# Optimization experiments

Measured on AMD Instinct MI355X. Metric: run time of the kernel, lower is better.

Reference implementation:

```python
import jax, jax.numpy as jnp
import numpy as np

B, S, D, H = 4, 2048, 1024, 16
DK = D // H


def setup_inputs() -> dict:
    key = jax.random.key(0)
    ks = jax.random.split(key, 12)
    std = 0.02
    inp = {
        "query": jax.random.normal(ks[0], (B, S, D), jnp.float32),
        "key": jax.random.normal(ks[1], (B, S, D), jnp.float32),
        "value": jax.random.normal(ks[2], (B, S, D), jnp.float32),
        "mask": jnp.ones((B, 1, 1, S), jnp.int32),
        "Wq": jax.random.normal(ks[3], (D, D), jnp.float32) * std,
        "bq": jnp.zeros((D,), jnp.float32),
        "Wk": jax.random.normal(ks[4], (D, D), jnp.float32) * std,
        "bk": jnp.zeros((D,), jnp.float32),
        "Wv": jax.random.normal(ks[5], (D, D), jnp.float32) * std,
        "bv": jnp.zeros((D,), jnp.float32),
        "Wo": jax.random.normal(ks[6], (D, D), jnp.float32) * std,
        "bo": jnp.zeros((D,), jnp.float32),
    }
    return inp


def reference(query, key, value, mask, Wq, bq, Wk, bk, Wv, bv, Wo, bo):
    # nn.Linear: x @ W.T + b; then split heads -> [B, H, S, DK]
    def proj(x, W, b):
        y = x @ W.T + b
        return y.reshape(B, S, H, DK).transpose(0, 2, 1, 3)

    q = proj(query, Wq, bq)
    k = proj(key, Wk, bk)
    v = proj(value, Wv, bv)

    scale = 1.0 / jnp.sqrt(jnp.asarray(DK, q.dtype))
    scores = jnp.einsum('bhqd,bhkd->bhqk', q, k) * scale  # [B,H,S,S]
    scores = jnp.where(mask == 0, jnp.asarray(-1e9, scores.dtype), scores)
    p_attn = jax.nn.softmax(scores, axis=-1)  # dropout p=0 -> identity
    ctx = jnp.einsum('bhqk,bhkd->bhqd', p_attn, v)
    ctx = ctx.transpose(0, 2, 1, 3).reshape(B, S, D)
    out = ctx @ Wo.T + bo
    return out
```

## Files before the change

### kernel.cpp

```cpp
#include <hip/hip_runtime.h>

#define BB 4
#define SS 2048
#define DD 1024
#define HH 16
#define DKC 64
#define MT (BB*SS)
#define NX (MT*DD)
#define NW (DD*DD)

typedef _Float16 f16x8 __attribute__((ext_vector_type(8)));
typedef _Float16 f16x4 __attribute__((ext_vector_type(4)));
typedef _Float16 f16x2 __attribute__((ext_vector_type(2)));
typedef float f32x4 __attribute__((ext_vector_type(4)));
typedef int   i32x4 __attribute__((ext_vector_type(4)));

__global__ __launch_bounds__(256) void cvt_all(const float* __restrict__ xq,
                                               const float* __restrict__ xk,
                                               const float* __restrict__ xv,
                                               const float* __restrict__ wq,
                                               const float* __restrict__ wk,
                                               const float* __restrict__ wv,
                                               const float* __restrict__ wo,
                                               _Float16* __restrict__ dst) {
  size_t i = ((size_t)blockIdx.x * 256 + threadIdx.x) * 4;
  const float* src; size_t off;
  if (i < (size_t)NX)          { src = xq; off = i; }
  else if (i < (size_t)2*NX)   { src = xk; off = i - (size_t)NX; }
  else if (i < (size_t)3*NX)   { src = xv; off = i - (size_t)2*NX; }
  else {
    size_t j = i - (size_t)3*NX;
    if (j < (size_t)NW)        { src = wq; off = j; }
    else if (j < (size_t)2*NW) { src = wk; off = j - (size_t)NW; }
    else if (j < (size_t)3*NW) { src = wv; off = j - (size_t)2*NW; }
    else                       { src = wo; off = j - (size_t)3*NW; }
  }
  f32x4 f = *(const f32x4*)(src + off);
  f16x4 o;
#pragma unroll
  for (int j = 0; j < 4; ++j) o[j] = (_Float16)f[j];
  *(f16x4*)(dst + i) = o;
}

__global__ __launch_bounds__(256) void gemm_qkv(const _Float16* __restrict__ Xb,
                                                const _Float16* __restrict__ Wb,
                                                const float* __restrict__ b0,
                                                const float* __restrict__ b1,
                                                const float* __restrict__ b2,
                                                _Float16* __restrict__ Pj) {
  const int z = blockIdx.z;
  const _Float16* A = Xb + (size_t)z * MT * DD;
  const _Float16* W = Wb + (size_t)z * DD * DD;
  const float* bias = (z == 0) ? b0 : ((z == 1) ? b1 : b2);
  _Float16* out = Pj + (size_t)z * MT * DD;

  const int m0 = blockIdx.x * 128;
  const int n0 = blockIdx.y * 128;
  const int t = threadIdx.x;
  const int lane = t & 63;
  const int wave = t >> 6;
  const int q = lane >> 4, r = lane & 15;
  const int wm = (wave & 1) * 64, wn = (wave >> 1) * 64;

  __shared__ __align__(16) _Float16 sA[128 * 32];
  __shared__ __align__(16) _Float16 sB[128 * 32];

  f32x4 acc[4][4] = {};

  const int row0 = t >> 2, cc = t & 3;

  f16x8 apre[2], bpre[2];
#pragma unroll
  for (int i = 0; i < 2; ++i) {
    int row = row0 + 64 * i;
    apre[i] = *(const f16x8*)(A + (size_t)(m0 + row) * DD + cc * 8);
    bpre[i] = *(const f16x8*)(W + (size_t)(n0 + row) * DD + cc * 8);
  }

  for (int k0 = 0; k0 < DD; k0 += 32) {
#pragma unroll
    for (int i = 0; i < 2; ++i) {
      int c = t + 256 * i;
      *(f16x8*)&sA[c * 8] = apre[i];
      *(f16x8*)&sB[c * 8] = bpre[i];
    }
    __syncthreads();

    if (k0 + 32 < DD) {
#pragma unroll
      for (int i = 0; i < 2; ++i) {
        int row = row0 + 64 * i;
        apre[i] = *(const f16x8*)(A + (size_t)(m0 + row) * DD + k0 + 32 + cc * 8);
        bpre[i] = *(const f16x8*)(W + (size_t)(n0 + row) * DD + k0 + 32 + cc * 8);
      }
    }

    f16x8 af[4], bf[4];
#pragma unroll
    for (int x = 0; x < 4; ++x) {
      af[x] = *(const f16x8*)&sA[(wm + x * 16 + r) * 32 + q * 8];
      bf[x] = *(const f16x8*)&sB[(wn + x * 16 + r) * 32 + q * 8];
    }
#pragma unroll
    for (int mi = 0; mi < 4; ++mi)
#pragma unroll
      for (int ni = 0; ni < 4; ++ni)
        acc[mi][ni] = __builtin_amdgcn_mfma_f32_16x16x32_f16(af[mi], bf[ni], acc[mi][ni], 0, 0, 0);
    __syncthreads();
  }

  if (z == 2) {
#pragma unroll
    for (int ni = 0; ni < 4; ++ni) {
      int gn = n0 + wn + ni * 16 + r;
      float bv = bias[gn];
      int h = gn >> 6, dk = gn & 63;
#pragma unroll
      for (int mi = 0; mi < 4; ++mi) {
        int gm = m0 + wm + mi * 16 + q * 4;
        int bb = gm >> 11, s0 = gm & 2047;
        int kl = s0 & 63;
        int kap0 = (kl & 15) * 4 + (kl >> 4);
        size_t base = ((size_t)((bb * HH + h) * DKC + dk)) * SS + (s0 - kl);
#pragma unroll
        for (int rr = 0; rr < 4; ++rr)
          out[base + kap0 + rr * 4] = (_Float16)(acc[mi][ni][rr] + bv);
      }
    }
  } else {
#pragma unroll
    for (int ni = 0; ni < 4; ++ni) {
      int gn = n0 + wn + ni * 16 + r;
      float bv = bias[gn];
      int h = gn >> 6, dk = gn & 63;
#pragma unroll
      for (int mi = 0; mi < 4; ++mi) {
#pragma unroll
        for (int rr = 0; rr < 4; ++rr) {
          int gm = m0 + wm + mi * 16 + q * 4 + rr;
          int bb = gm >> 11, s = gm & 2047;
          out[((size_t)((bb * HH + h) * SS + s)) * DKC + dk] = (_Float16)(acc[mi][ni][rr] + bv);
        }
      }
    }
  }
}

__global__ __launch_bounds__(256) void attn(const _Float16* __restrict__ Pj,
                                            const int* __restrict__ mask,
                                            _Float16* __restrict__ Cx) {
  const int qt = blockIdx.x, h = blockIdx.y, bb = blockIdx.z;
  const size_t hoff = ((size_t)(bb * HH + h) * SS) * DKC;
  const _Float16* Qh  = Pj + hoff;
  const _Float16* Kh  = Pj + (size_t)MT * DD + hoff;
  const _Float16* Vth = Pj + (size_t)2 * MT * DD + hoff;
  _Float16* Ch = Cx + hoff;
  const int* mrow = mask + bb * SS;

  const int t = threadIdx.x, lane = t & 63, wave = t >> 6;
  const int q = lane >> 4, r = lane & 15;
  const int qrow0 = qt * 128 + wave * 32;

  __shared__ __align__(16) _Float16 sK[64 * 64];
  __shared__ __align__(16) _Float16 sVt[64 * 64];
  __shared__ __align__(16) _Float16 sP[4][32 * 64];
  __shared__ __align__(16) float    sMB[SS];

  {
    int i0 = t * 8;
    i32x4 m0v = *(const i32x4*)(mrow + i0);
    i32x4 m1v = *(const i32x4*)(mrow + i0 + 4);
    f32x4 b0v, b1v;
#pragma unroll
    for (int j = 0; j < 4; ++j) {
      b0v[j] = m0v[j] ? 0.0f : -1e30f;
      b1v[j] = m1v[j] ? 0.0f : -1e30f;
    }
    *(f32x4*)&sMB[i0] = b0v;
    *(f32x4*)&sMB[i0 + 4] = b1v;
  }

  f16x8 qf[2][2];
#pragma unroll
  for (int mi = 0; mi < 2; ++mi)
#pragma unroll
    for (int kk = 0; kk < 2; ++kk)
      qf[mi][kk] = *(const f16x8*)&Qh[(size_t)(qrow0 + mi * 16 + r) * DKC + kk * 32 + q * 8];

  float lst[2][4] = {};
  f32x4 oacc[2][4] = {};

  const float C2 = 0.125f * 1.44269504089f;

  const int srow0 = t >> 3, scc = t & 7;

  f16x8 kpre[2], vpre[2];
#pragma unroll
  for (int i = 0; i < 2; ++i) {
    int row = srow0 + 32 * i;
    kpre[i] = *(const f16x8*)(Kh + (size_t)row * DKC + scc * 8);
    vpre[i] = *(const f16x8*)(Vth + (size_t)row * SS + scc * 8);
  }

  for (int kt = 0; kt < SS; kt += 64) {
#pragma unroll
    for (int i = 0; i < 2; ++i) {
      int row = srow0 + 32 * i;
      *(f16x8*)&sK [row * 64 + ((scc ^ (row & 7)) << 3)]        = kpre[i];
      *(f16x8*)&sVt[row * 64 + ((scc ^ ((row & 1) << 2)) << 3)] = vpre[i];
    }
    __syncthreads();

    if (kt + 64 < SS) {
#pragma unroll
      for (int i = 0; i < 2; ++i) {
        int row = srow0 + 32 * i;
        kpre[i] = *(const f16x8*)(Kh + (size_t)(kt + 64 + row) * DKC + scc * 8);
        vpre[i] = *(const f16x8*)(Vth + (size_t)row * SS + kt + 64 + scc * 8);
      }
    }

    f32x4 sacc[2][4] = {};
#pragma unroll
    for (int kk = 0; kk < 2; ++kk) {
      f16x8 kb[4];
#pragma unroll
      for (int ni = 0; ni < 4; ++ni)
        kb[ni] = *(const f16x8*)&sK[(ni * 16 + r) * 64 + ((((kk * 4 + q) ^ (r & 7)) << 3))];
#pragma unroll
      for (int mi = 0; mi < 2; ++mi)
#pragma unroll
        for (int ni = 0; ni < 4; ++ni)
          sacc[mi][ni] = __builtin_amdgcn_mfma_f32_16x16x32_f16(qf[mi][kk], kb[ni], sacc[mi][ni], 0, 0, 0);
    }

    float mb[4];
#pragma unroll
    for (int ni = 0; ni < 4; ++ni) mb[ni] = sMB[kt + ni * 16 + r];

#pragma unroll
    for (int mi = 0; mi < 2; ++mi) {
#pragma unroll
      for (int rr = 0; rr < 4; ++rr) {
        float pp[4];
#pragma unroll
        for (int ni = 0; ni < 4; ++ni)
          pp[ni] = __builtin_amdgcn_exp2f(__builtin_fmaf(sacc[mi][ni][rr], C2, mb[ni]));
        lst[mi][rr] += (pp[0] + pp[1]) + (pp[2] + pp[3]);
        int prow = mi * 16 + q * 4 + rr;
        int goff = prow * 64 + (((r >> 1) ^ ((rr & 1) << 2)) << 3) + ((r & 1) << 2);
        unsigned lo = __builtin_bit_cast(unsigned, __builtin_amdgcn_cvt_pkrtz(pp[0], pp[1]));
        unsigned hi = __builtin_bit_cast(unsigned, __builtin_amdgcn_cvt_pkrtz(pp[2], pp[3]));
        uint2 u; u.x = lo; u.y = hi;
        *(uint2*)&sP[wave][goff] = u;
      }
    }
    __threadfence_block();

#pragma unroll
    for (int kk = 0; kk < 2; ++kk) {
      f16x8 ap[2], vb[4];
#pragma unroll
      for (int mi = 0; mi < 2; ++mi) {
        int row = mi * 16 + r;
        int g = ((kk * 4 + q) ^ ((r & 1) << 2)) << 3;
        ap[mi] = *(const f16x8*)&sP[wave][row * 64 + g];
      }
#pragma unroll
      for (int ni = 0; ni < 4; ++ni) {
        int row = ni * 16 + r;
        int g = ((kk * 4 + q) ^ ((r & 1) << 2)) << 3;
        vb[ni] = *(const f16x8*)&sVt[row * 64 + g];
      }
#pragma unroll
      for (int mi = 0; mi < 2; ++mi)
#pragma unroll
        for (int ni = 0; ni < 4; ++ni)
          oacc[mi][ni] = __builtin_amdgcn_mfma_f32_16x16x32_f16(ap[mi], vb[ni], oacc[mi][ni], 0, 0, 0);
    }
    __syncthreads();
  }

#pragma unroll
  for (int mi = 0; mi < 2; ++mi)
#pragma unroll
    for (int rr = 0; rr < 4; ++rr) {
      float l = lst[mi][rr];
#pragma unroll
      for (int d = 1; d < 16; d <<= 1) l += __shfl_xor(l, d);
      lst[mi][rr] = 1.0f / l;
    }

#pragma unroll
  for (int mi = 0; mi < 2; ++mi)
#pragma unroll
    for (int ni = 0; ni < 4; ++ni)
#pragma unroll
      for (int rr = 0; rr < 4; ++rr) {
        int row = qrow0 + mi * 16 + q * 4 + rr;
        Ch[(size_t)row * DKC + ni * 16 + r] = (_Float16)(oacc[mi][ni][rr] * lst[mi][rr]);
      }
}

__global__ __launch_bounds__(256) void gemm_out(const _Float16* __restrict__ Cx,
                                                const _Float16* __restrict__ W,
                                                const float* __restrict__ bias,
                                                float* __restrict__ out) {
  const int m0 = blockIdx.x * 128;
  const int n0 = blockIdx.y * 128;
  const int t = threadIdx.x;
  const int lane = t & 63;
  const int wave = t >> 6;
  const int q = lane >> 4, r = lane & 15;
  const int wm = (wave & 1) * 64, wn = (wave >> 1) * 64;

  __shared__ __align__(16) _Float16 sA[128 * 32];
  __shared__ __align__(16) _Float16 sB[128 * 32];

  f32x4 acc[4][4] = {};

  const int row0 = t >> 2, cc = t & 3;
  size_t abase[2];
#pragma unroll
  for (int i = 0; i < 2; ++i) {
    int gm = m0 + row0 + 64 * i;
    int bb = gm >> 11, s = gm & 2047;
    abase[i] = ((size_t)(bb * HH) * SS + s) * DKC;
  }

  f16x8 apre[2], bpre[2];
#pragma unroll
  for (int i = 0; i < 2; ++i) {
    apre[i] = *(const f16x8*)(Cx + abase[i] + cc * 8);
    bpre[i] = *(const f16x8*)(W + (size_t)(n0 + row0 + 64 * i) * DD + cc * 8);
  }

  for (int k0 = 0; k0 < DD; k0 += 32) {
#pragma unroll
    for (int i = 0; i < 2; ++i) {
      int c = t + 256 * i;
      *(f16x8*)&sA[c * 8] = apre[i];
      *(f16x8*)&sB[c * 8] = bpre[i];
    }
    __syncthreads();

    if (k0 + 32 < DD) {
      int k1 = k0 + 32;
      int head = k1 >> 6, off = (k1 & 63) + cc * 8;
#pragma unroll
      for (int i = 0; i < 2; ++i) {
        apre[i] = *(const f16x8*)(Cx + abase[i] + (size_t)head * SS * DKC + off);
        bpre[i] = *(const f16x8*)(W + (size_t)(n0 + row0 + 64 * i) * DD + k1 + cc * 8);
      }
    }

    f16x8 af[4], bf[4];
#pragma unroll
    for (int x = 0; x < 4; ++x) {
      af[x] = *(const f16x8*)&sA[(wm + x * 16 + r) * 32 + q * 8];
      bf[x] = *(const f16x8*)&sB[(wn + x * 16 + r) * 32 + q * 8];
    }
#pragma unroll
    for (int mi = 0; mi < 4; ++mi)
#pragma unroll
      for (int ni = 0; ni < 4; ++ni)
        acc[mi][ni] = __builtin_amdgcn_mfma_f32_16x16x32_f16(af[mi], bf[ni], acc[mi][ni], 0, 0, 0);
    __syncthreads();
  }

#pragma unroll
  for (int ni = 0; ni < 4; ++ni) {
    int gn = n0 + wn + ni * 16 + r;
    float bv = bias[gn];
#pragma unroll
    for (int mi = 0; mi < 4; ++mi) {
#pragma unroll
      for (int rr = 0; rr < 4; ++rr) {
        int gm = m0 + wm + mi * 16 + q * 4 + rr;
        out[(size_t)gm * DD + gn] = acc[mi][ni][rr] + bv;
      }
    }
  }
}

extern "C" void kernel_launch(void* const* d_in, const int* in_sizes, int n_in,
                              void* d_out, int out_size, void* d_ws, size_t ws_size,
                              hipStream_t stream) {
  const float* query = (const float*)d_in[0];
  const float* key_  = (const float*)d_in[1];
  const float* value = (const float*)d_in[2];
  const int*   mask  = (const int*)d_in[3];
  const float* Wq = (const float*)d_in[4];
  const float* bq = (const float*)d_in[5];
  const float* Wk = (const float*)d_in[6];
  const float* bk = (const float*)d_in[7];
  const float* Wv = (const float*)d_in[8];
  const float* bv = (const float*)d_in[9];
  const float* Wo = (const float*)d_in[10];
  const float* bo = (const float*)d_in[11];
  float* out = (float*)d_out;

  _Float16* Xb = (_Float16*)d_ws;
  _Float16* Wb = Xb + (size_t)3 * NX;
  _Float16* Pj = Wb + (size_t)4 * NW;
  _Float16* Cx = Pj + (size_t)3 * NX;

  cvt_all<<<(3 * NX + 4 * NW) / 1024, 256, 0, stream>>>(query, key_, value, Wq, Wk, Wv, Wo, Xb);

  gemm_qkv<<<dim3(MT / 128, DD / 128, 3), 256, 0, stream>>>(Xb, Wb, bq, bk, bv, Pj);
  attn<<<dim3(SS / 128, HH, BB), 256, 0, stream>>>(Pj, mask, Cx);
  gemm_out<<<dim3(MT / 128, DD / 128), 256, 0, stream>>>(Cx, Wb + (size_t)3 * NW, bo, out);
}
```

Before: 370.9 us.

## Use direct global-to-LDS double-buffered loads, swizzled LDS, setprio and fp16 mask bias

Both GEMM kernels replace the register-staged prefetch with global_load_lds direct-to-shared loads into a double buffer, using an XOR swizzle on the column chunk to avoid LDS bank conflicts. The attention kernel unifies the LDS swizzle for V and P to an 8-way XOR pattern, wraps MFMA blocks with s_setprio to favour matrix issue, and stores the mask bias as fp16 to halve its LDS footprint. This aims to cut VGPR pressure, LDS store instructions and bank conflicts. The risks are the correctness of the swizzle mapping and that the fp16 -30000 mask value behaves differently from -1e30.

```diff
diff --git a/kernel.cpp b/kernel.cpp
--- a/kernel.cpp
+++ b/kernel.cpp
@@ -11,9 +11,13 @@
 
 typedef _Float16 f16x8 __attribute__((ext_vector_type(8)));
 typedef _Float16 f16x4 __attribute__((ext_vector_type(4)));
-typedef _Float16 f16x2 __attribute__((ext_vector_type(2)));
 typedef float f32x4 __attribute__((ext_vector_type(4)));
 typedef int   i32x4 __attribute__((ext_vector_type(4)));
+
+#define GLDS16(g, l)                                                         \
+  __builtin_amdgcn_global_load_lds(                                          \
+      (__attribute__((address_space(1))) void*)(g),                          \
+      (__attribute__((address_space(3))) void*)(l), 16, 0, 0)
 
 __global__ __launch_bounds__(256) void cvt_all(const float* __restrict__ xq,
                                                const float* __restrict__ xk,
@@ -62,44 +66,37 @@
   const int q = lane >> 4, r = lane & 15;
   const int wm = (wave & 1) * 64, wn = (wave >> 1) * 64;
 
-  __shared__ __align__(16) _Float16 sA[128 * 32];
-  __shared__ __align__(16) _Float16 sB[128 * 32];
+  __shared__ __align__(16) _Float16 sA[2][128 * 32];
+  __shared__ __align__(16) _Float16 sB[2][128 * 32];
 
   f32x4 acc[4][4] = {};
 
-  const int row0 = t >> 2, cc = t & 3;
-
-  f16x8 apre[2], bpre[2];
-#pragma unroll
-  for (int i = 0; i < 2; ++i) {
-    int row = row0 + 64 * i;
-    apre[i] = *(const f16x8*)(A + (size_t)(m0 + row) * DD + cc * 8);
-    bpre[i] = *(const f16x8*)(W + (size_t)(n0 + row) * DD + cc * 8);
-  }
-
+  const int row0 = t >> 2;
+  const int csw = (t & 3) ^ ((t >> 3) & 3);
+  const int fsw = (r >> 1) & 3;
+
+  auto stage = [&](int buf, int k0) {
+#pragma unroll
+    for (int i = 0; i < 2; ++i) {
+      GLDS16(A + (size_t)(m0 + row0 + 64 * i) * DD + k0 + csw * 8,
+             &sA[buf][(t + 256 * i) * 8]);
+      GLDS16(W + (size_t)(n0 + row0 + 64 * i) * DD + k0 + csw * 8,
+             &sB[buf][(t + 256 * i) * 8]);
+    }
+  };
+
+  stage(0, 0);
+  __syncthreads();
+
+  int cur = 0;
   for (int k0 = 0; k0 < DD; k0 += 32) {
-#pragma unroll
-    for (int i = 0; i < 2; ++i) {
-      int c = t + 256 * i;
-      *(f16x8*)&sA[c * 8] = apre[i];
-      *(f16x8*)&sB[c * 8] = bpre[i];
-    }
-    __syncthreads();
-
-    if (k0 + 32 < DD) {
-#pragma unroll
-      for (int i = 0; i < 2; ++i) {
-        int row = row0 + 64 * i;
-        apre[i] = *(const f16x8*)(A + (size_t)(m0 + row) * DD + k0 + 32 + cc * 8);
-        bpre[i] = *(const f16x8*)(W + (size_t)(n0 + row) * DD + k0 + 32 + cc * 8);
-      }
-    }
+    if (k0 + 32 < DD) stage(cur ^ 1, k0 + 32);
 
     f16x8 af[4], bf[4];
 #pragma unroll
     for (int x = 0; x < 4; ++x) {
-      af[x] = *(const f16x8*)&sA[(wm + x * 16 + r) * 32 + q * 8];
-      bf[x] = *(const f16x8*)&sB[(wn + x * 16 + r) * 32 + q * 8];
+      af[x] = *(const f16x8*)&sA[cur][(wm + x * 16 + r) * 32 + ((q ^ fsw) * 8)];
+      bf[x] = *(const f16x8*)&sB[cur][(wn + x * 16 + r) * 32 + ((q ^ fsw) * 8)];
     }
 #pragma unroll
     for (int mi = 0; mi < 4; ++mi)
@@ -107,6 +104,7 @@
       for (int ni = 0; ni < 4; ++ni)
         acc[mi][ni] = __builtin_amdgcn_mfma_f32_16x16x32_f16(af[mi], bf[ni], acc[mi][ni], 0, 0, 0);
     __syncthreads();
+    cur ^= 1;
   }
 
   if (z == 2) {
@@ -164,20 +162,19 @@
   __shared__ __align__(16) _Float16 sK[64 * 64];
   __shared__ __align__(16) _Float16 sVt[64 * 64];
   __shared__ __align__(16) _Float16 sP[4][32 * 64];
-  __shared__ __align__(16) float    sMB[SS];
+  __shared__ __align__(16) _Float16 sMBh[SS];
 
   {
     int i0 = t * 8;
     i32x4 m0v = *(const i32x4*)(mrow + i0);
     i32x4 m1v = *(const i32x4*)(mrow + i0 + 4);
-    f32x4 b0v, b1v;
+    f16x8 bvv;
 #pragma unroll
     for (int j = 0; j < 4; ++j) {
-      b0v[j] = m0v[j] ? 0.0f : -1e30f;
-      b1v[j] = m1v[j] ? 0.0f : -1e30f;
-    }
-    *(f32x4*)&sMB[i0] = b0v;
-    *(f32x4*)&sMB[i0 + 4] = b1v;
+      bvv[j]     = m0v[j] ? (_Float16)0.0f : (_Float16)(-30000.0f);
+      bvv[4 + j] = m1v[j] ? (_Float16)0.0f : (_Float16)(-30000.0f);
+    }
+    *(f16x8*)&sMBh[i0] = bvv;
   }
 
   f16x8 qf[2][2];
@@ -206,8 +203,8 @@
 #pragma unroll
     for (int i = 0; i < 2; ++i) {
       int row = srow0 + 32 * i;
-      *(f16x8*)&sK [row * 64 + ((scc ^ (row & 7)) << 3)]        = kpre[i];
-      *(f16x8*)&sVt[row * 64 + ((scc ^ ((row & 1) << 2)) << 3)] = vpre[i];
+      *(f16x8*)&sK [row * 64 + ((scc ^ (row & 7)) << 3)] = kpre[i];
+      *(f16x8*)&sVt[row * 64 + ((scc ^ (row & 7)) << 3)] = vpre[i];
     }
     __syncthreads();
 
@@ -226,17 +223,19 @@
       f16x8 kb[4];
 #pragma unroll
       for (int ni = 0; ni < 4; ++ni)
-        kb[ni] = *(const f16x8*)&sK[(ni * 16 + r) * 64 + ((((kk * 4 + q) ^ (r & 7)) << 3))];
+        kb[ni] = *(const f16x8*)&sK[(ni * 16 + r) * 64 + (((kk * 4 + q) ^ (r & 7)) << 3)];
+      __builtin_amdgcn_s_setprio(1);
 #pragma unroll
       for (int mi = 0; mi < 2; ++mi)
 #pragma unroll
         for (int ni = 0; ni < 4; ++ni)
           sacc[mi][ni] = __builtin_amdgcn_mfma_f32_16x16x32_f16(qf[mi][kk], kb[ni], sacc[mi][ni], 0, 0, 0);
+      __builtin_amdgcn_s_setprio(0);
     }
 
     float mb[4];
 #pragma unroll
-    for (int ni = 0; ni < 4; ++ni) mb[ni] = sMB[kt + ni * 16 + r];
+    for (int ni = 0; ni < 4; ++ni) mb[ni] = (float)sMBh[kt + ni * 16 + r];
 
 #pragma unroll
     for (int mi = 0; mi < 2; ++mi) {
@@ -248,7 +247,8 @@
           pp[ni] = __builtin_amdgcn_exp2f(__builtin_fmaf(sacc[mi][ni][rr], C2, mb[ni]));
         lst[mi][rr] += (pp[0] + pp[1]) + (pp[2] + pp[3]);
         int prow = mi * 16 + q * 4 + rr;
-        int goff = prow * 64 + (((r >> 1) ^ ((rr & 1) << 2)) << 3) + ((r & 1) << 2);
+        int g = (r >> 1) ^ ((q * 4 + rr) & 7);
+        int goff = prow * 64 + (g << 3) + ((r & 1) << 2);
         unsigned lo = __builtin_bit_cast(unsigned, __builtin_amdgcn_cvt_pkrtz(pp[0], pp[1]));
         unsigned hi = __builtin_bit_cast(unsigned, __builtin_amdgcn_cvt_pkrtz(pp[2], pp[3]));
         uint2 u; u.x = lo; u.y = hi;
@@ -261,22 +261,18 @@
     for (int kk = 0; kk < 2; ++kk) {
       f16x8 ap[2], vb[4];
 #pragma unroll
-      for (int mi = 0; mi < 2; ++mi) {
-        int row = mi * 16 + r;
-        int g = ((kk * 4 + q) ^ ((r & 1) << 2)) << 3;
-        ap[mi] = *(const f16x8*)&sP[wave][row * 64 + g];
-      }
-#pragma unroll
-      for (int ni = 0; ni < 4; ++ni) {
-        int row = ni * 16 + r;
-        int g = ((kk * 4 + q) ^ ((r & 1) << 2)) << 3;
-        vb[ni] = *(const f16x8*)&sVt[row * 64 + g];
-      }
+      for (int mi = 0; mi < 2; ++mi)
+        ap[mi] = *(const f16x8*)&sP[wave][(mi * 16 + r) * 64 + (((kk * 4 + q) ^ (r & 7)) << 3)];
+#pragma unroll
+      for (int ni = 0; ni < 4; ++ni)
+        vb[ni] = *(const f16x8*)&sVt[(ni * 16 + r) * 64 + (((kk * 4 + q) ^ (r & 7)) << 3)];
+      __builtin_amdgcn_s_setprio(1);
 #pragma unroll
       for (int mi = 0; mi < 2; ++mi)
 #pragma unroll
         for (int ni = 0; ni < 4; ++ni)
           oacc[mi][ni] = __builtin_amdgcn_mfma_f32_16x16x32_f16(ap[mi], vb[ni], oacc[mi][ni], 0, 0, 0);
+      __builtin_amdgcn_s_setprio(0);
     }
     __syncthreads();
   }
@@ -314,12 +310,15 @@
   const int q = lane >> 4, r = lane & 15;
   const int wm = (wave & 1) * 64, wn = (wave >> 1) * 64;
 
-  __shared__ __align__(16) _Float16 sA[128 * 32];
-  __shared__ __align__(16) _Float16 sB[128 * 32];
+  __shared__ __align__(16) _Float16 sA[2][128 * 32];
+  __shared__ __align__(16) _Float16 sB[2][128 * 32];
 
   f32x4 acc[4][4] = {};
 
-  const int row0 = t >> 2, cc = t & 3;
+  const int row0 = t >> 2;
+  const int csw = (t & 3) ^ ((t >> 3) & 3);
+  const int fsw = (r >> 1) & 3;
+
   size_t abase[2];
 #pragma unroll
   for (int i = 0; i < 2; ++i) {
@@ -328,37 +327,29 @@
     abase[i] = ((size_t)(bb * HH) * SS + s) * DKC;
   }
 
-  f16x8 apre[2], bpre[2];
-#pragma unroll
-  for (int i = 0; i < 2; ++i) {
-    apre[i] = *(const f16x8*)(Cx + abase[i] + cc * 8);
-    bpre[i] = *(const f16x8*)(W + (size_t)(n0 + row0 + 64 * i) * DD + cc * 8);
-  }
-
+  auto stage = [&](int buf, int k0) {
+    int head = k0 >> 6, off = (k0 & 63) + csw * 8;
+#pragma unroll
+    for (int i = 0; i < 2; ++i) {
+      GLDS16(Cx + abase[i] + (size_t)head * SS * DKC + off,
+             &sA[buf][(t + 256 * i) * 8]);
+      GLDS16(W + (size_t)(n0 + row0 + 64 * i) * DD + k0 + csw * 8,
+             &sB[buf][(t + 256 * i) * 8]);
+    }
+  };
+
+  stage(0, 0);
+  __syncthreads();
+
+  int cur = 0;
   for (int k0 = 0; k0 < DD; k0 += 32) {
-#pragma unroll
-    for (int i = 0; i < 2; ++i) {
-      int c = t + 256 * i;
-      *(f16x8*)&sA[c * 8] = apre[i];
-      *(f16x8*)&sB[c * 8] = bpre[i];
-    }
-    __syncthreads();
-
-    if (k0 + 32 < DD) {
-      int k1 = k0 + 32;
-      int head = k1 >> 6, off = (k1 & 63) + cc * 8;
-#pragma unroll
-      for (int i = 0; i < 2; ++i) {
-        apre[i] = *(const f16x8*)(Cx + abase[i] + (size_t)head * SS * DKC + off);
-        bpre[i] = *(const f16x8*)(W + (size_t)(n0 + row0 + 64 * i) * DD + k1 + cc * 8);
-      }
-    }
+    if (k0 + 32 < DD) stage(cur ^ 1, k0 + 32);
 
     f16x8 af[4], bf[4];
 #pragma unroll
     for (int x = 0; x < 4; ++x) {
-      af[x] = *(const f16x8*)&sA[(wm + x * 16 + r) * 32 + q * 8];
-      bf[x] = *(const f16x8*)&sB[(wn + x * 16 + r) * 32 + q * 8];
+      af[x] = *(const f16x8*)&sA[cur][(wm + x * 16 + r) * 32 + ((q ^ fsw) * 8)];
+      bf[x] = *(const f16x8*)&sB[cur][(wn + x * 16 + r) * 32 + ((q ^ fsw) * 8)];
     }
 #pragma unroll
     for (int mi = 0; mi < 4; ++mi)
@@ -366,6 +357,7 @@
       for (int ni = 0; ni < 4; ++ni)
         acc[mi][ni] = __builtin_amdgcn_mfma_f32_16x16x32_f16(af[mi], bf[ni], acc[mi][ni], 0, 0, 0);
     __syncthreads();
+    cur ^= 1;
   }
 
 #pragma unroll
```

Result: no change. 363.6 us (-2.0%).
